# Performance work log

Hardware: AMD Instinct MI355X
Metric: run time of the kernel (lower is better)

The kernel has to match this reference:

```python
import jax, jax.numpy as jnp
import numpy as np

# Basis ordering for PGA(3,0,1), matching GATr / the module's index tables
# (original_id/shifted_id/flip_sign_id correspond to right-multiplication by e0):
# 0:1  1:e0  2:e1  3:e2  4:e3  5:e01 6:e02 7:e03 8:e12 9:e13 10:e23
# 11:e012 12:e013 13:e023 14:e123 15:e0123
_BLADES = [(), (0,), (1,), (2,), (3,), (0, 1), (0, 2), (0, 3), (1, 2), (1, 3), (2, 3),
           (0, 1, 2), (0, 1, 3), (0, 2, 3), (1, 2, 3), (0, 1, 2, 3)]
_BITS = [sum(1 << e for e in b) for b in _BLADES]
_IDX_OF_BITS = {bits: i for i, bits in enumerate(_BITS)}


def _sign_cat(a, b):
    # (-1)^(number of transpositions to sort the concatenated basis lists)
    swaps = 0
    a >>= 1
    while a:
        swaps += bin(a & b).count('1')
        a >>= 1
    return -1.0 if swaps & 1 else 1.0


def _build_tables():
    geom = np.zeros((16, 16, 16), np.float32)
    wedge = np.zeros((16, 16, 16), np.float32)
    for i, a in enumerate(_BITS):
        for j, b in enumerate(_BITS):
            k = _IDX_OF_BITS[a ^ b]
            s = _sign_cat(a, b)
            if (a & b) == 0:                 # disjoint blades: geometric == wedge
                geom[i, j, k] = s
                wedge[i, j, k] = s
            elif not (a & b & 1):            # e1,e2,e3 square to +1; e0^2 = 0
                geom[i, j, k] = s
    return geom, wedge


_GEOM_NP, _WEDGE_NP = _build_tables()
GEOM = jnp.asarray(_GEOM_NP)
WEDGE = jnp.asarray(_WEDGE_NP)
E0_RIGHT = jnp.asarray(_GEOM_NP[:, 1, :])    # x -> x * e0 (index shuffle + sign flips)

_gm = np.zeros((5, 16), np.float32)          # GRADE_MASK[k, m] = 1 iff blade m has grade k
for _i, _b in enumerate(_BLADES):
    _gm[len(_b), _i] = 1.0
GRADE_MASK = jnp.asarray(_gm)

# Poincare dual: e_i ^ e_complement(i) = DUAL_SIGN[i] * e0123; complement index = 15 - i
DUAL_SIGN = jnp.asarray(np.array([_sign_cat(a, 0b1111 ^ a) for a in _BITS], np.float32))


def dual(x):
    return (x * DUAL_SIGN)[..., ::-1]


def equi_linear(x, w):
    # x: [b, s, c, 16], w: [C, c, 9]
    blade = x[..., None, :] * GRADE_MASK                              # [b,s,c,5,16]
    blade_e0 = jnp.einsum('...ki,ij->...kj', blade[..., :4, :], E0_RIGHT)  # [b,s,c,4,16]
    combined = jnp.concatenate([blade, blade_e0], axis=-2)            # [b,s,c,9,16]
    # Faithful to original torch.einsum('bsckm,Ccn->bsCm', ...):
    # k and n are DIFFERENT labels, so each is summed independently.
    return jnp.einsum('bsckm,Ccn->bsCm', combined, w)


def table_prod(x, y, table):
    return jnp.einsum('...i,...j,ijm->...m', x, y, table)


def reference(x, w_join_x, w_join_y, w_geom_x, w_geom_y):
    z = jnp.mean(x, axis=(0, 1, 2))           # [16] reference multivector
    z = z.at[:15].set(0.0)                    # Z[:-1] = 0: keep only e0123 component
    Xj = equi_linear(x, w_join_x)
    Yj = equi_linear(x, w_join_y)
    Xg = equi_linear(x, w_geom_x)
    Yg = equi_linear(x, w_geom_y)
    line = table_prod(dual(Xj), dual(Yj), WEDGE)          # X* ^ Y*
    join = jnp.einsum('i,...j,ijm->...m', z, dual(line), GEOM)  # Z[e0123] * (X*^Y*)*
    geom = table_prod(Xg, Yg, GEOM)
    return jnp.concatenate([join, geom], axis=-2)         # [b, s, out_channels, 16]


def setup_inputs():
    key = jax.random.key(0)
    ks = jax.random.split(key, 5)
    B, S, C_IN, C_OUT = 4, 4096, 32, 64
    half = C_OUT // 2
    x = jax.random.normal(ks[0], (B, S, C_IN, 16), jnp.float32)
    names = ['w_join_x', 'w_join_y', 'w_geom_x', 'w_geom_y']
    ws = {n: jax.random.normal(k, (half, C_IN, 9), jnp.float32) for n, k in zip(names, ks[1:])}
    return {'x': x, **ws}
```

## Files before the change

kernel.cpp:

```cpp
#include <hip/hip_runtime.h>
#include <utility>
#include <cstddef>

#define NROWS 16384
#define CIN 32
#define X15_N (NROWS*CIN)
#define POSB 8
#define RED_BLOCKS 1024
#define PART_OFF 256
#define W_OFF 1536

constexpr int BITS_[16] = {0,1,2,4,8,3,5,9,6,10,12,7,11,13,14,15};

constexpr int idx_of(int bits) { int r = -1; for (int i = 0; i < 16; ++i) if (BITS_[i] == bits) r = i; return r; }

constexpr int sign_cat(int a, int b) {
  int sw = 0; a >>= 1;
  while (a) { sw += __builtin_popcount(a & b); a >>= 1; }
  return (sw & 1) ? -1 : 1;
}

constexpr int ds_(int i) { return sign_cat(BITS_[i], 15 ^ BITS_[i]); }

constexpr int geom_s(int i, int j) { int a = BITS_[i], b = BITS_[j]; return ((a & b & 1) == 0) ? sign_cat(a, b) : 0; }
constexpr int geom_m(int i, int j) { return idx_of(BITS_[i] ^ BITS_[j]); }

constexpr int tj_s(int i, int j) {
  int pa = BITS_[15 - i], qa = BITS_[15 - j];
  if (pa & qa) return 0;
  int m1 = idx_of(pa ^ qa);
  int jb = BITS_[15 - m1];
  if (jb & 1) return 0;
  return ds_(i) * ds_(j) * sign_cat(pa, qa) * ds_(m1) * sign_cat(15, jb);
}
constexpr int tj_m(int i, int j) {
  int pa = BITS_[15 - i], qa = BITS_[15 - j];
  int m1 = idx_of(pa ^ qa);
  int jb = BITS_[15 - m1];
  return idx_of(15 ^ jb);
}

template <int I, int J>
__device__ __forceinline__ void accum_pair(float (&g)[16], float (&jn)[16],
    const float (&xg)[16], const float (&yg)[16],
    const float (&xj)[16], const float (&yj)[16]) {
  constexpr int gs = geom_s(I, J);
  if constexpr (gs != 0) {
    constexpr int m = geom_m(I, J);
    if constexpr (gs > 0) g[m] = fmaf(xg[I],  yg[J], g[m]);
    else                  g[m] = fmaf(xg[I], -yg[J], g[m]);
  }
  constexpr int js = tj_s(I, J);
  if constexpr (js != 0) {
    constexpr int m = tj_m(I, J);
    if constexpr (js > 0) jn[m] = fmaf(xj[I],  yj[J], jn[m]);
    else                  jn[m] = fmaf(xj[I], -yj[J], jn[m]);
  }
}

template <size_t... P>
__device__ __forceinline__ void accum_all(float (&g)[16], float (&jn)[16],
    const float (&xg)[16], const float (&yg)[16],
    const float (&xj)[16], const float (&yj)[16], std::index_sequence<P...>) {
  (accum_pair<(int)(P / 16), (int)(P % 16)>(g, jn, xg, yg, xj, yj), ...);
}

__global__ __launch_bounds__(256) void reduce_x15(const float* __restrict__ x, float* __restrict__ partials) {
  __shared__ float red[256];
  float s = 0.f;
  for (int i = blockIdx.x * 256 + threadIdx.x; i < X15_N; i += 256 * RED_BLOCKS)
    s += x[(long)i * 16 + 15];
  red[threadIdx.x] = s;
  __syncthreads();
  for (int off = 128; off > 0; off >>= 1) {
    if (threadIdx.x < off) red[threadIdx.x] += red[threadIdx.x + off];
    __syncthreads();
  }
  if (threadIdx.x == 0) partials[blockIdx.x] = red[0];
}

__global__ __launch_bounds__(256) void prep(const float* __restrict__ partials,
                                            const float* __restrict__ wjx, const float* __restrict__ wjy,
                                            const float* __restrict__ wgx, const float* __restrict__ wgy,
                                            float* __restrict__ wsv) {
  __shared__ float red[256];
  const int tid = threadIdx.x;
  red[tid] = partials[tid] + partials[tid + 256] + partials[tid + 512] + partials[tid + 768];
  __syncthreads();
  for (int off = 128; off > 0; off >>= 1) {
    if (tid < off) red[tid] += red[tid + off];
    __syncthreads();
  }
  if (tid == 0) wsv[0] = red[0] * (1.0f / (float)X15_N);

  for (int f = tid; f < CIN * 4 * 32; f += 256) {
    const int cc = f >> 7, v = (f >> 5) & 3, C = f & 31;
    const float* w = (v == 0) ? wjx : (v == 1) ? wjy : (v == 2) ? wgx : wgy;
    const float* wp = w + ((size_t)C * CIN + cc) * 9;
    float s = 0.f;
#pragma unroll
    for (int n = 0; n < 9; ++n) s += wp[n];
    wsv[W_OFF + f] = s;
  }
}

__global__ __launch_bounds__(256) void ga_main(const float* __restrict__ x,
                                               const float* __restrict__ wsv,
                                               float* __restrict__ out) {
  __shared__ float sW[CIN][4][32];
  __shared__ float sU[POSB][CIN][16];

  const int tid = threadIdx.x;

  const float* wsrc = wsv + W_OFF;
#pragma unroll
  for (int f = tid; f < CIN * 4 * 32; f += 256)
    (&sW[0][0][0])[f] = wsrc[f];

  const int pos = tid >> 5;
  const int lc  = tid & 31;
  const long row = (long)blockIdx.x * POSB + pos;
  const float4* xp = (const float4*)(x + (row * CIN + lc) * 16);
  const float4 a0 = xp[0], a1 = xp[1], a2 = xp[2], a3 = xp[3];
  float4 u0, u1, u2, u3;
  u0.x = a0.x;         u0.y = a0.y + a0.x;  u0.z = a0.z;         u0.w = a0.w;
  u1.x = a1.x;         u1.y = a1.y - a0.z;  u1.z = a1.z - a0.w;  u1.w = a1.w - a1.x;
  u2.x = a2.x;         u2.y = a2.y;         u2.z = a2.z;         u2.w = a2.w + a2.x;
  u3.x = a3.x + a2.y;  u3.y = a3.y + a2.z;  u3.z = a3.z;         u3.w = a3.w - a3.z;
  float4* up = (float4*)&sU[pos][lc][0];
  up[0] = u0; up[1] = u1; up[2] = u2; up[3] = u3;

  const float z15 = wsv[0];
  __syncthreads();

  const int C = lc;
  float xj[16], yj[16], xg[16], yg[16];
#pragma unroll
  for (int m = 0; m < 16; ++m) { xj[m] = 0.f; yj[m] = 0.f; xg[m] = 0.f; yg[m] = 0.f; }

  const float* sWb = &sW[0][0][0] + C;
  const float4* sUb = (const float4*)&sU[pos][0][0];

#define GSTEP(idx, val) \
    xj[idx] = fmaf(w0, (val), xj[idx]); \
    yj[idx] = fmaf(w1, (val), yj[idx]); \
    xg[idx] = fmaf(w2, (val), xg[idx]); \
    yg[idx] = fmaf(w3, (val), yg[idx]);

#pragma unroll 4
  for (int cc = 0; cc < CIN; ++cc) {
    const float w0 = sWb[cc * 128];
    const float w1 = sWb[cc * 128 + 32];
    const float w2 = sWb[cc * 128 + 64];
    const float w3 = sWb[cc * 128 + 96];
    const float4 v0 = sUb[cc * 4 + 0];
    const float4 v1 = sUb[cc * 4 + 1];
    const float4 v2 = sUb[cc * 4 + 2];
    const float4 v3 = sUb[cc * 4 + 3];
    GSTEP(0,  v0.x) GSTEP(1,  v0.y) GSTEP(2,  v0.z) GSTEP(3,  v0.w)
    GSTEP(4,  v1.x) GSTEP(5,  v1.y) GSTEP(6,  v1.z) GSTEP(7,  v1.w)
    GSTEP(8,  v2.x) GSTEP(9,  v2.y) GSTEP(10, v2.z) GSTEP(11, v2.w)
    GSTEP(12, v3.x) GSTEP(13, v3.y) GSTEP(14, v3.z) GSTEP(15, v3.w)
  }
#undef GSTEP

  float g[16], jn[16];
#pragma unroll
  for (int m = 0; m < 16; ++m) { g[m] = 0.f; jn[m] = 0.f; }
  accum_all(g, jn, xg, yg, xj, yj, std::make_index_sequence<256>{});
#pragma unroll
  for (int m = 0; m < 16; ++m) jn[m] *= z15;

  float* ob = out + (row * 64 + C) * 16;
  float4* oj = (float4*)ob;
  oj[0] = make_float4(jn[0],  jn[1],  jn[2],  jn[3]);
  oj[1] = make_float4(jn[4],  jn[5],  jn[6],  jn[7]);
  oj[2] = make_float4(jn[8],  jn[9],  jn[10], jn[11]);
  oj[3] = make_float4(jn[12], jn[13], jn[14], jn[15]);
  float4* og = (float4*)(ob + 32 * 16);
  og[0] = make_float4(g[0],  g[1],  g[2],  g[3]);
  og[1] = make_float4(g[4],  g[5],  g[6],  g[7]);
  og[2] = make_float4(g[8],  g[9],  g[10], g[11]);
  og[3] = make_float4(g[12], g[13], g[14], g[15]);
}

extern "C" void kernel_launch(void* const* d_in, const int* in_sizes, int n_in,
                              void* d_out, int out_size, void* d_ws, size_t ws_size,
                              hipStream_t stream) {
  const float* x   = (const float*)d_in[0];
  const float* wjx = (const float*)d_in[1];
  const float* wjy = (const float*)d_in[2];
  const float* wgx = (const float*)d_in[3];
  const float* wgy = (const float*)d_in[4];
  float* out = (float*)d_out;
  float* wsv = (float*)d_ws;

  reduce_x15<<<RED_BLOCKS, 256, 0, stream>>>(x, wsv + PART_OFF);
  prep<<<1, 256, 0, stream>>>(wsv + PART_OFF, wjx, wjy, wgx, wgy, wsv);
  ga_main<<<NROWS / POSB, 256, 0, stream>>>(x, wsv, out);
}
```

Baseline: 70.14 us.

## Compute equi-linear projection with split-bf16 MFMA instead of scalar FMAs

Replaces the per-thread scalar FMA loop for the four channel-mixing projections with MFMA 16x16x32 bf16 matrix instructions. Precision is kept close to fp32 by splitting operands into high and low bf16 parts and summing three products. Results pass through a swizzled shared-memory buffer before the per-thread geometric and join products, which now run in two passes. The weights are re-laid out in prep to suit the new layout. This adds bf16 conversion work, extra shared memory and extra barriers, and is slightly less accurate than fp32.

```diff
diff --git a/kernel.cpp b/kernel.cpp
--- a/kernel.cpp
+++ b/kernel.cpp
@@ -10,6 +10,9 @@
 #define PART_OFF 256
 #define W_OFF 1536
 
+typedef float f32x4 __attribute__((ext_vector_type(4)));
+typedef short bf16x8 __attribute__((ext_vector_type(8)));
+
 constexpr int BITS_[16] = {0,1,2,4,8,3,5,9,6,10,12,7,11,13,14,15};
 
 constexpr int idx_of(int bits) { int r = -1; for (int i = 0; i < 16; ++i) if (BITS_[i] == bits) r = i; return r; }
@@ -41,28 +44,38 @@
 }
 
 template <int I, int J>
-__device__ __forceinline__ void accum_pair(float (&g)[16], float (&jn)[16],
-    const float (&xg)[16], const float (&yg)[16],
-    const float (&xj)[16], const float (&yj)[16]) {
+__device__ __forceinline__ void acc_geom(float (&g)[16], const float (&x)[16], const float (&y)[16]) {
   constexpr int gs = geom_s(I, J);
   if constexpr (gs != 0) {
     constexpr int m = geom_m(I, J);
-    if constexpr (gs > 0) g[m] = fmaf(xg[I],  yg[J], g[m]);
-    else                  g[m] = fmaf(xg[I], -yg[J], g[m]);
-  }
+    if constexpr (gs > 0) g[m] = fmaf(x[I],  y[J], g[m]);
+    else                  g[m] = fmaf(x[I], -y[J], g[m]);
+  }
+}
+template <int I, int J>
+__device__ __forceinline__ void acc_join(float (&g)[16], const float (&x)[16], const float (&y)[16]) {
   constexpr int js = tj_s(I, J);
   if constexpr (js != 0) {
     constexpr int m = tj_m(I, J);
-    if constexpr (js > 0) jn[m] = fmaf(xj[I],  yj[J], jn[m]);
-    else                  jn[m] = fmaf(xj[I], -yj[J], jn[m]);
-  }
-}
-
+    if constexpr (js > 0) g[m] = fmaf(x[I],  y[J], g[m]);
+    else                  g[m] = fmaf(x[I], -y[J], g[m]);
+  }
+}
 template <size_t... P>
-__device__ __forceinline__ void accum_all(float (&g)[16], float (&jn)[16],
-    const float (&xg)[16], const float (&yg)[16],
-    const float (&xj)[16], const float (&yj)[16], std::index_sequence<P...>) {
-  (accum_pair<(int)(P / 16), (int)(P % 16)>(g, jn, xg, yg, xj, yj), ...);
+__device__ __forceinline__ void all_geom(float (&g)[16], const float (&x)[16], const float (&y)[16], std::index_sequence<P...>) {
+  (acc_geom<(int)(P / 16), (int)(P % 16)>(g, x, y), ...);
+}
+template <size_t... P>
+__device__ __forceinline__ void all_join(float (&g)[16], const float (&x)[16], const float (&y)[16], std::index_sequence<P...>) {
+  (acc_join<(int)(P / 16), (int)(P % 16)>(g, x, y), ...);
+}
+
+__device__ __forceinline__ unsigned short f2bf(float f) {
+  unsigned int b = __float_as_uint(f);
+  return (unsigned short)((b + 0x7FFFu + ((b >> 16) & 1u)) >> 16);
+}
+__device__ __forceinline__ float bf2f(unsigned short h) {
+  return __uint_as_float(((unsigned int)h) << 16);
 }
 
 __global__ __launch_bounds__(256) void reduce_x15(const float* __restrict__ x, float* __restrict__ partials) {
@@ -93,8 +106,8 @@
   }
   if (tid == 0) wsv[0] = red[0] * (1.0f / (float)X15_N);
 
-  for (int f = tid; f < CIN * 4 * 32; f += 256) {
-    const int cc = f >> 7, v = (f >> 5) & 3, C = f & 31;
+  for (int f = tid; f < 4096; f += 256) {
+    const int v = f >> 10, C = (f >> 5) & 31, cc = f & 31;
     const float* w = (v == 0) ? wjx : (v == 1) ? wjy : (v == 2) ? wgx : wgy;
     const float* wp = w + ((size_t)C * CIN + cc) * 9;
     float s = 0.f;
@@ -107,81 +120,128 @@
 __global__ __launch_bounds__(256) void ga_main(const float* __restrict__ x,
                                                const float* __restrict__ wsv,
                                                float* __restrict__ out) {
-  __shared__ float sW[CIN][4][32];
-  __shared__ float sU[POSB][CIN][16];
+  __shared__ unsigned short sWh[128][32];
+  __shared__ unsigned short sWl[128][32];
+  __shared__ unsigned short sUh[POSB][16][32];
+  __shared__ unsigned short sUl[POSB][16][32];
+  __shared__ float sB[POSB][32][2][16];
 
   const int tid = threadIdx.x;
-
-  const float* wsrc = wsv + W_OFF;
-#pragma unroll
-  for (int f = tid; f < CIN * 4 * 32; f += 256)
-    (&sW[0][0][0])[f] = wsrc[f];
+  const float z15 = wsv[0];
+
+  {
+    const float* wsrc = wsv + W_OFF;
+    unsigned short* wh = &sWh[0][0];
+    unsigned short* wl = &sWl[0][0];
+#pragma unroll
+    for (int f = tid; f < 4096; f += 256) {
+      const float s = wsrc[f];
+      const unsigned short h = f2bf(s);
+      wh[f] = h;
+      wl[f] = f2bf(s - bf2f(h));
+    }
+  }
 
   const int pos = tid >> 5;
-  const int lc  = tid & 31;
-  const long row = (long)blockIdx.x * POSB + pos;
-  const float4* xp = (const float4*)(x + (row * CIN + lc) * 16);
-  const float4 a0 = xp[0], a1 = xp[1], a2 = xp[2], a3 = xp[3];
-  float4 u0, u1, u2, u3;
-  u0.x = a0.x;         u0.y = a0.y + a0.x;  u0.z = a0.z;         u0.w = a0.w;
-  u1.x = a1.x;         u1.y = a1.y - a0.z;  u1.z = a1.z - a0.w;  u1.w = a1.w - a1.x;
-  u2.x = a2.x;         u2.y = a2.y;         u2.z = a2.z;         u2.w = a2.w + a2.x;
-  u3.x = a3.x + a2.y;  u3.y = a3.y + a2.z;  u3.z = a3.z;         u3.w = a3.w - a3.z;
-  float4* up = (float4*)&sU[pos][lc][0];
-  up[0] = u0; up[1] = u1; up[2] = u2; up[3] = u3;
-
-  const float z15 = wsv[0];
+  const int c = tid & 31;
+  const long row0 = (long)blockIdx.x * POSB;
+  {
+    const float4* xp = (const float4*)(x + ((row0 + pos) * CIN + c) * 16);
+    const float4 a0 = xp[0], a1 = xp[1], a2 = xp[2], a3 = xp[3];
+    float u[16];
+    u[0]  = a0.x;        u[1]  = a0.y + a0.x; u[2]  = a0.z;        u[3]  = a0.w;
+    u[4]  = a1.x;        u[5]  = a1.y - a0.z; u[6]  = a1.z - a0.w; u[7]  = a1.w - a1.x;
+    u[8]  = a2.x;        u[9]  = a2.y;        u[10] = a2.z;        u[11] = a2.w + a2.x;
+    u[12] = a3.x + a2.y; u[13] = a3.y + a2.z; u[14] = a3.z;        u[15] = a3.w - a3.z;
+#pragma unroll
+    for (int m = 0; m < 16; ++m) {
+      const unsigned short h = f2bf(u[m]);
+      sUh[pos][m][c] = h;
+      sUl[pos][m][c] = f2bf(u[m] - bf2f(h));
+    }
+  }
   __syncthreads();
 
-  const int C = lc;
-  float xj[16], yj[16], xg[16], yg[16];
-#pragma unroll
-  for (int m = 0; m < 16; ++m) { xj[m] = 0.f; yj[m] = 0.f; xg[m] = 0.f; yg[m] = 0.f; }
-
-  const float* sWb = &sW[0][0][0] + C;
-  const float4* sUb = (const float4*)&sU[pos][0][0];
-
-#define GSTEP(idx, val) \
-    xj[idx] = fmaf(w0, (val), xj[idx]); \
-    yj[idx] = fmaf(w1, (val), yj[idx]); \
-    xg[idx] = fmaf(w2, (val), xg[idx]); \
-    yg[idx] = fmaf(w3, (val), yg[idx]);
-
-#pragma unroll 4
-  for (int cc = 0; cc < CIN; ++cc) {
-    const float w0 = sWb[cc * 128];
-    const float w1 = sWb[cc * 128 + 32];
-    const float w2 = sWb[cc * 128 + 64];
-    const float w3 = sWb[cc * 128 + 96];
-    const float4 v0 = sUb[cc * 4 + 0];
-    const float4 v1 = sUb[cc * 4 + 1];
-    const float4 v2 = sUb[cc * 4 + 2];
-    const float4 v3 = sUb[cc * 4 + 3];
-    GSTEP(0,  v0.x) GSTEP(1,  v0.y) GSTEP(2,  v0.z) GSTEP(3,  v0.w)
-    GSTEP(4,  v1.x) GSTEP(5,  v1.y) GSTEP(6,  v1.z) GSTEP(7,  v1.w)
-    GSTEP(8,  v2.x) GSTEP(9,  v2.y) GSTEP(10, v2.z) GSTEP(11, v2.w)
-    GSTEP(12, v3.x) GSTEP(13, v3.y) GSTEP(14, v3.z) GSTEP(15, v3.w)
-  }
-#undef GSTEP
-
-  float g[16], jn[16];
-#pragma unroll
-  for (int m = 0; m < 16; ++m) { g[m] = 0.f; jn[m] = 0.f; }
-  accum_all(g, jn, xg, yg, xj, yj, std::make_index_sequence<256>{});
-#pragma unroll
-  for (int m = 0; m < 16; ++m) jn[m] *= z15;
-
-  float* ob = out + (row * 64 + C) * 16;
-  float4* oj = (float4*)ob;
-  oj[0] = make_float4(jn[0],  jn[1],  jn[2],  jn[3]);
-  oj[1] = make_float4(jn[4],  jn[5],  jn[6],  jn[7]);
-  oj[2] = make_float4(jn[8],  jn[9],  jn[10], jn[11]);
-  oj[3] = make_float4(jn[12], jn[13], jn[14], jn[15]);
-  float4* og = (float4*)(ob + 32 * 16);
-  og[0] = make_float4(g[0],  g[1],  g[2],  g[3]);
-  og[1] = make_float4(g[4],  g[5],  g[6],  g[7]);
-  og[2] = make_float4(g[8],  g[9],  g[10], g[11]);
-  og[3] = make_float4(g[12], g[13], g[14], g[15]);
+  const int lane = tid & 63;
+  const int w = tid >> 6;
+  const int lm = lane & 15;
+  const int lk = lane >> 4;
+  const int p0 = 2 * w, p1 = 2 * w + 1;
+
+#pragma unroll
+  for (int pass = 0; pass < 2; ++pass) {
+    bf16x8 bh[4], bl[4];
+#pragma unroll
+    for (int t = 0; t < 4; ++t) {
+      bh[t] = *(const bf16x8*)&sWh[pass * 64 + t * 16 + lm][lk * 8];
+      bl[t] = *(const bf16x8*)&sWl[pass * 64 + t * 16 + lm][lk * 8];
+    }
+    const bf16x8 ah0 = *(const bf16x8*)&sUh[p0][lm][lk * 8];
+    const bf16x8 al0 = *(const bf16x8*)&sUl[p0][lm][lk * 8];
+    const bf16x8 ah1 = *(const bf16x8*)&sUh[p1][lm][lk * 8];
+    const bf16x8 al1 = *(const bf16x8*)&sUl[p1][lm][lk * 8];
+
+    f32x4 d0[4], d1[4];
+#pragma unroll
+    for (int t = 0; t < 4; ++t) {
+      const f32x4 zz = {0.f, 0.f, 0.f, 0.f};
+      f32x4 m0 = __builtin_amdgcn_mfma_f32_16x16x32_bf16(ah0, bh[t], zz, 0, 0, 0);
+      f32x4 c0a = __builtin_amdgcn_mfma_f32_16x16x32_bf16(ah0, bl[t], zz, 0, 0, 0);
+      f32x4 c0b = __builtin_amdgcn_mfma_f32_16x16x32_bf16(al0, bh[t], zz, 0, 0, 0);
+      d0[t] = m0 + c0a + c0b;
+      f32x4 m1 = __builtin_amdgcn_mfma_f32_16x16x32_bf16(ah1, bh[t], zz, 0, 0, 0);
+      f32x4 c1a = __builtin_amdgcn_mfma_f32_16x16x32_bf16(ah1, bl[t], zz, 0, 0, 0);
+      f32x4 c1b = __builtin_amdgcn_mfma_f32_16x16x32_bf16(al1, bh[t], zz, 0, 0, 0);
+      d1[t] = m1 + c1a + c1b;
+    }
+
+#pragma unroll
+    for (int t = 0; t < 4; ++t) {
+      const int Cw = (t & 1) * 16 + lm;
+      const int vw = t >> 1;
+      const int slot = lk ^ (Cw & 3);
+      *(f32x4*)&sB[p0][Cw][vw][slot * 4] = d0[t];
+      *(f32x4*)&sB[p1][Cw][vw][slot * 4] = d1[t];
+    }
+    __syncthreads();
+
+    float xv[16], yv[16];
+#pragma unroll
+    for (int s = 0; s < 4; ++s) {
+      const int mq = s ^ (c & 3);
+      f32x4 qx = *(const f32x4*)&sB[pos][c][0][s * 4];
+      f32x4 qy = *(const f32x4*)&sB[pos][c][1][s * 4];
+#pragma unroll
+      for (int e = 0; e < 4; ++e) { xv[mq * 4 + e] = qx[e]; yv[mq * 4 + e] = qy[e]; }
+    }
+
+    float r[16];
+#pragma unroll
+    for (int m = 0; m < 16; ++m) r[m] = 0.f;
+
+    if (pass == 0) {
+      all_join(r, xv, yv, std::make_index_sequence<256>{});
+      float* ob = out + (((row0 + pos) * 64) + c) * 16;
+      f32x4 o;
+#pragma unroll
+      for (int q = 0; q < 4; ++q) {
+#pragma unroll
+        for (int e = 0; e < 4; ++e) o[e] = r[q * 4 + e] * z15;
+        *(f32x4*)(ob + q * 4) = o;
+      }
+    } else {
+      all_geom(r, xv, yv, std::make_index_sequence<256>{});
+      float* ob = out + (((row0 + pos) * 64) + 32 + c) * 16;
+      f32x4 o;
+#pragma unroll
+      for (int q = 0; q < 4; ++q) {
+#pragma unroll
+        for (int e = 0; e < 4; ++e) o[e] = r[q * 4 + e];
+        *(f32x4*)(ob + q * 4) = o;
+      }
+    }
+    __syncthreads();
+  }
 }
 
 extern "C" void kernel_launch(void* const* d_in, const int* in_sizes, int n_in,
```

Result: slower. 77.58 us (+10.6%).
